# Optimization experiments

Hardware: AMD Instinct MI355X
Metric: run time of the kernel (lower is better)

The kernel has to match this reference:

```python
import jax, jax.numpy as jnp
import numpy as np

N = 50000   # nodes
D = 128     # input_dim
E = 1600000 # edges
K = 100     # out_nodes


def setup_inputs() -> dict:
    key = jax.random.key(0)
    ks = jax.random.split(key, 9)
    x = jax.random.normal(ks[0], (N, D), dtype=jnp.float32)
    edge_index = jax.random.randint(ks[1], (2, E), 0, N, dtype=jnp.int64)
    # PyG GCNConv params: Linear(in,out,bias=False) weight + separate bias
    s = 1.0 / np.sqrt(D)
    W1 = jax.random.uniform(ks[2], (D, D), jnp.float32, -s, s)
    b1 = jnp.zeros((D,), jnp.float32)
    W2 = jax.random.uniform(ks[3], (D, D), jnp.float32, -s, s)
    b2 = jnp.zeros((D,), jnp.float32)
    Wa = jax.random.uniform(ks[4], (D, K), jnp.float32, -s, s)
    ba = jax.random.uniform(ks[5], (K,), jnp.float32, -s, s)
    return {"x": x, "edge_index": edge_index, "W1": W1, "b1": b1,
            "W2": W2, "b2": b2, "Wa": Wa, "ba": ba}


def _gcn_conv(x, src, dst, norm, W, b, n_nodes):
    # PyG GCNConv: h = x @ W; aggregate D^-1/2 (A+I) D^-1/2 h; add bias
    h = x @ W                                  # [N, D]
    msg = h[src] * norm[:, None]               # [E+N, D] gather + scale
    agg = jax.ops.segment_sum(msg, dst, num_segments=n_nodes)  # scatter-add
    return agg + b


def reference(x, edge_index, W1, b1, W2, b2, Wa, ba):
    n = x.shape[0]
    loop = jnp.arange(n, dtype=edge_index.dtype)
    src = jnp.concatenate([edge_index[0], loop])   # add self-loops
    dst = jnp.concatenate([edge_index[1], loop])
    deg = jnp.zeros((n,), x.dtype).at[dst].add(1.0)
    dinv = jnp.where(deg > 0, jax.lax.rsqrt(deg), 0.0)
    norm = dinv[src] * dinv[dst]                   # [E+N]

    h = _gcn_conv(x, src, dst, norm, W1, b1, n)
    h = jax.nn.relu(h)
    h = _gcn_conv(h, src, dst, norm, W2, b2, n)
    s = jax.nn.softmax(h @ Wa + ba, axis=1)        # [N, K]
    return s
```

## Files before the change

kernel.cpp:

```cpp
#include <hip/hip_runtime.h>

#define D 128
#define KOUT 100
#define CHUNK 4096

typedef __attribute__((ext_vector_type(8))) short short8;
typedef __attribute__((ext_vector_type(4))) float floatx4;

__device__ inline float bf_lo(unsigned int u) { return __uint_as_float(u << 16); }
__device__ inline float bf_hi(unsigned int u) { return __uint_as_float(u & 0xFFFF0000u); }

__device__ inline unsigned int bf_round(float a) {
    unsigned int ua = __float_as_uint(a);
    return (ua + 0x7FFFu + ((ua >> 16) & 1u)) >> 16;
}
__device__ inline unsigned int pack_bf(float a, float b) {
    return bf_round(a) | (bf_round(b) << 16);
}


__launch_bounds__(256)
__global__ void bucket_pass1(const int* __restrict__ ei, int E, int nbuck, int cap,
                             int* __restrict__ bcur, unsigned int* __restrict__ bdata) {
    __shared__ int hist[256];
    __shared__ int sc[256];
    __shared__ int pfx[256];
    __shared__ int cur[256];
    __shared__ int gbase[256];
    __shared__ unsigned int lbuf[CHUNK];
    __shared__ unsigned char bkt[CHUNK];

    int tid = threadIdx.x;
    int base = blockIdx.x * CHUNK;
    int cnt = E - base; if (cnt > CHUNK) cnt = CHUNK;

    hist[tid] = 0;
    __syncthreads();

    int src[CHUNK / 256];
    int dst[CHUNK / 256];
#pragma unroll
    for (int q = 0; q < CHUNK / 256; q++) {
        int li = tid + q * 256;
        if (li < cnt) {
            src[q] = ei[base + li];
            dst[q] = ei[E + base + li];
            atomicAdd(&hist[dst[q] >> 8], 1);
        }
    }
    __syncthreads();

    int v = hist[tid];
    sc[tid] = v;
    __syncthreads();
    for (int off = 1; off < 256; off <<= 1) {
        int t = (tid >= off) ? sc[tid - off] : 0;
        __syncthreads();
        sc[tid] += t;
        __syncthreads();
    }
    int excl = sc[tid] - v;
    pfx[tid] = excl;
    cur[tid] = excl;
    gbase[tid] = 0;
    if (tid < nbuck && v > 0) gbase[tid] = atomicAdd(&bcur[tid], v);
    __syncthreads();

#pragma unroll
    for (int q = 0; q < CHUNK / 256; q++) {
        int li = tid + q * 256;
        if (li < cnt) {
            int b = dst[q] >> 8;
            int p = atomicAdd(&cur[b], 1);
            lbuf[p] = (unsigned int)src[q] | ((unsigned int)(dst[q] & 255) << 24);
            bkt[p] = (unsigned char)b;
        }
    }
    __syncthreads();

    for (int p = tid; p < cnt; p += 256) {
        int b = bkt[p];
        bdata[(size_t)b * cap + gbase[b] + (p - pfx[b])] = lbuf[p];
    }
}


__launch_bounds__(256)
__global__ void bucket_build(const unsigned int* __restrict__ bdata, const int* __restrict__ bcur,
                             int cap, float* __restrict__ dinv,
                             int* __restrict__ rowptr, int* __restrict__ csr, int n, int nbuck) {
    __shared__ int cnts[256];
    __shared__ int sc[256];
    __shared__ int cur[256];
    __shared__ int bbase;

    int b = blockIdx.x, tid = threadIdx.x;
    if (tid == 0) bbase = 0;
    cnts[tid] = 0;
    __syncthreads();

    int part = 0;
    for (int t = tid; t < b; t += 256) part += bcur[t];
#pragma unroll
    for (int off = 32; off > 0; off >>= 1) part += __shfl_down(part, off);
    if ((tid & 63) == 0 && part != 0) atomicAdd(&bbase, part);

    int cnt = bcur[b];
    const unsigned int* p = bdata + (size_t)b * cap;
    for (int e = tid; e < cnt; e += 256) atomicAdd(&cnts[p[e] >> 24], 1);
    __syncthreads();

    int v = cnts[tid];
    sc[tid] = v;
    __syncthreads();
    for (int off = 1; off < 256; off <<= 1) {
        int t = (tid >= off) ? sc[tid - off] : 0;
        __syncthreads();
        sc[tid] += t;
        __syncthreads();
    }
    int gstart = bbase + (sc[tid] - v);
    int node = b * 256 + tid;
    if (node < n) {
        dinv[node] = rsqrtf((float)(v + 1));
        rowptr[node] = gstart;
    }
    cur[tid] = gstart;
    __syncthreads();

    for (int e = tid; e < cnt; e += 256) {
        unsigned int u = p[e];
        int pos = atomicAdd(&cur[u >> 24], 1);
        csr[pos] = (int)(u & 0xFFFFFFu);
    }
}


__global__ void prep_frag_kernel(const float* __restrict__ W1, const float* __restrict__ W2,
                                 const float* __restrict__ Wa, const float* __restrict__ ba,
                                 unsigned short* __restrict__ Wf1, unsigned short* __restrict__ Wf2,
                                 unsigned short* __restrict__ WfA, float* __restrict__ bpad,
                                 int* __restrict__ bcur, int* __restrict__ rowptr,
                                 unsigned int* __restrict__ zrowA, unsigned int* __restrict__ zrowB,
                                 int n, int E) {
    int idx = blockIdx.x * blockDim.x + threadIdx.x;
    if (idx < 3 * 16384) {
        int m = idx / 16384;
        int e = idx & 16383;
        int j = e & 7, lane = (e >> 3) & 63, ct = (e >> 9) & 7, kt = e >> 12;
        int k = kt * 32 + (lane >> 4) * 8 + j;
        int col = ct * 16 + (lane & 15);
        float val;
        unsigned short* dst;
        if (m == 0)      { val = W1[k * 128 + col]; dst = Wf1; }
        else if (m == 1) { val = W2[k * 128 + col]; dst = Wf2; }
        else             { val = (col < KOUT) ? Wa[k * KOUT + col] : 0.f; dst = WfA; }
        dst[e] = (unsigned short)bf_round(val);
    }
    if (idx < 128) bpad[idx] = (idx < KOUT) ? ba[idx] : 0.f;
    if (idx < 256) bcur[idx] = 0;
    if (idx < 64) { zrowA[idx] = 0u; zrowB[idx] = 0u; }
    if (idx == 256) rowptr[n] = E;
}


__launch_bounds__(256)
__global__ void gemm_mfma_kernel(const void* __restrict__ Xin, const unsigned short* __restrict__ Wf,
                                 const float* __restrict__ bias, const float* __restrict__ oscale,
                                 void* __restrict__ Y, int nrows, int in_bf16, int out_mode) {
    __shared__ float lds_f[64 * 130];
    unsigned short* lds_h = (unsigned short*)lds_f;
    unsigned int* lds_u = (unsigned int*)lds_f;

    int tid = threadIdx.x;
    int w = tid >> 6, lane = tid & 63;
    int quad = lane >> 4, m16 = lane & 15;
    int r0 = blockIdx.x * 64;

    if (!in_bf16) {
        int row = tid >> 2, cg_ = tid & 3;
        bool valid = (r0 + row) < nrows;
        const float4* Xr = (const float4*)Xin + (size_t)(r0 + row) * 32 + cg_ * 8;
#pragma unroll
        for (int j = 0; j < 8; j++) {
            float4 v = valid ? Xr[j] : make_float4(0.f, 0.f, 0.f, 0.f);
            int c = cg_ * 32 + j * 4;
            lds_u[row * 68 + (c >> 1)]     = pack_bf(v.x, v.y);
            lds_u[row * 68 + (c >> 1) + 1] = pack_bf(v.z, v.w);
        }
        __syncthreads();
    }

    floatx4 acc[8];
#pragma unroll
    for (int ct = 0; ct < 8; ct++) acc[ct] = (floatx4){0.f, 0.f, 0.f, 0.f};

    int arow = r0 + w * 16 + m16;
    if (arow > nrows - 1) arow = nrows - 1;
    const unsigned int* Xb = (const unsigned int*)Xin;

    const short8* Wf8 = (const short8*)Wf;
#pragma unroll
    for (int kt = 0; kt < 4; kt++) {
        short8 a;
        if (in_bf16) {
            a = *(const short8*)(Xb + (size_t)arow * 64 + kt * 16 + quad * 4);
        } else {
            a = *(const short8*)(lds_h + (w * 16 + m16) * 136 + kt * 32 + quad * 8);
        }
#pragma unroll
        for (int ct = 0; ct < 8; ct++) {
            short8 b = Wf8[(kt * 8 + ct) * 64 + lane];
            acc[ct] = __builtin_amdgcn_mfma_f32_16x16x32_bf16(a, b, acc[ct], 0, 0, 0);
        }
    }

    if (out_mode == 1) {
        __syncthreads();
#pragma unroll
        for (int ct = 0; ct < 8; ct++) {
#pragma unroll
            for (int r = 0; r < 4; r++) {
                int rl = w * 16 + quad * 4 + r;
                lds_f[rl * 130 + ct * 16 + m16] = acc[ct][r];
            }
        }
        __syncthreads();
        unsigned int* Yb = (unsigned int*)Y;
        for (int r = 0; r < 16; r++) {
            int row = r0 + w * 16 + r;
            if (row < nrows) {
                float sc = oscale ? oscale[row] : 1.f;
                float lo = lds_f[(w * 16 + r) * 130 + 2 * lane] * sc;
                float hi = lds_f[(w * 16 + r) * 130 + 2 * lane + 1] * sc;
                Yb[(size_t)row * 64 + lane] = pack_bf(lo, hi);
            }
        }
    } else {
        float bb[8];
#pragma unroll
        for (int ct = 0; ct < 8; ct++) bb[ct] = bias[ct * 16 + m16];
        float* Yf = (float*)Y;
#pragma unroll
        for (int r = 0; r < 4; r++) {
            int row = r0 + w * 16 + quad * 4 + r;
            float vv[8];
            float mx = -1e30f;
#pragma unroll
            for (int ct = 0; ct < 8; ct++) {
                int col = ct * 16 + m16;
                vv[ct] = (col < KOUT) ? acc[ct][r] + bb[ct] : -1e30f;
                mx = fmaxf(mx, vv[ct]);
            }
#pragma unroll
            for (int off = 1; off < 16; off <<= 1) mx = fmaxf(mx, __shfl_xor(mx, off));
            float se = 0.f;
#pragma unroll
            for (int ct = 0; ct < 8; ct++) {
                vv[ct] = (vv[ct] > -1e29f) ? __expf(vv[ct] - mx) : 0.f;
                se += vv[ct];
            }
#pragma unroll
            for (int off = 1; off < 16; off <<= 1) se += __shfl_xor(se, off);
            float inv = 1.f / se;
            if (row < nrows) {
#pragma unroll
                for (int ct = 0; ct < 8; ct++) {
                    int col = ct * 16 + m16;
                    if (col < KOUT) Yf[(size_t)row * KOUT + col] = vv[ct] * inv;
                }
            }
        }
    }
}


__launch_bounds__(256)
__global__ void aggregate_kernel(const uint4* __restrict__ Hb4, const int* __restrict__ csr,
                                 const int* __restrict__ rowptr,
                                 const float* __restrict__ dinv, const float* __restrict__ bias,
                                 unsigned int* __restrict__ Ob, int n, int do_relu) {
    int wid = threadIdx.x >> 6, lane = threadIdx.x & 63;
    int g = lane >> 4, c = lane & 15;
    int i = blockIdx.x * 4 + wid;
    if (i >= n) return;

    float di = dinv[i];
    int start = rowptr[i];
    int cnt = rowptr[i + 1] - start;
    const int* cp = csr + start;

    float acc[8];
    {
        uint4 sv = Hb4[(size_t)i * 16 + c];
        unsigned int su[4] = {sv.x, sv.y, sv.z, sv.w};
        if (g != 0) { su[0] = su[1] = su[2] = su[3] = 0u; }
#pragma unroll
        for (int t = 0; t < 4; t++) {
            acc[2 * t]     = bf_lo(su[t]);
            acc[2 * t + 1] = bf_hi(su[t]);
        }
    }

    int s[4];
#pragma unroll
    for (int u = 0; u < 4; u++) {
        int idx = u * 4 + g;
        s[u] = (idx < cnt) ? cp[idx] : n;
    }
    for (int e = 0; e < cnt; e += 16) {
        uint4 v[4];
#pragma unroll
        for (int u = 0; u < 4; u++) v[u] = Hb4[(size_t)s[u] * 16 + c];
        int ns[4];
#pragma unroll
        for (int u = 0; u < 4; u++) {
            int idx = e + 16 + u * 4 + g;
            ns[u] = (idx < cnt) ? cp[idx] : n;
        }
#pragma unroll
        for (int u = 0; u < 4; u++) {
            unsigned int uu[4] = {v[u].x, v[u].y, v[u].z, v[u].w};
#pragma unroll
            for (int t = 0; t < 4; t++) {
                acc[2 * t]     += bf_lo(uu[t]);
                acc[2 * t + 1] += bf_hi(uu[t]);
            }
        }
#pragma unroll
        for (int u = 0; u < 4; u++) s[u] = ns[u];
    }

#pragma unroll
    for (int j = 0; j < 8; j++) {
        acc[j] += __shfl_xor(acc[j], 16);
        acc[j] += __shfl_xor(acc[j], 32);
    }

    float2 bb = ((const float2*)bias)[c * 4 + g];
    float fx = acc[g * 2]     * di + bb.x;
    float fy = acc[g * 2 + 1] * di + bb.y;
    if (do_relu) { fx = fmaxf(fx, 0.f); fy = fmaxf(fy, 0.f); }
    Ob[(size_t)i * 64 + c * 4 + g] = pack_bf(fx, fy);
}


extern "C" void kernel_launch(void* const* d_in, const int* in_sizes, int n_in,
                              void* d_out, int out_size, void* d_ws, size_t ws_size,
                              hipStream_t stream) {
    const float* x  = (const float*)d_in[0];
    const int*   ei = (const int*)d_in[1];
    const float* W1 = (const float*)d_in[2];
    const float* b1 = (const float*)d_in[3];
    const float* W2 = (const float*)d_in[4];
    const float* b2 = (const float*)d_in[5];
    const float* Wa = (const float*)d_in[6];
    const float* ba = (const float*)d_in[7];
    float* out = (float*)d_out;

    int N = in_sizes[0] / D;
    int E = in_sizes[1] / 2;

    int nbuck = (N + 255) >> 8;
    int cap = ((E / nbuck) + 2048 + 63) & ~63;

    char* w = (char*)d_ws;
    size_t off = 0;
    auto carve = [&](size_t bytes) -> void* {
        void* p = w + off;
        off = (off + bytes + 255) & ~(size_t)255;
        return p;
    };
    float* dinv   = (float*)carve((size_t)N * 4);
    int*   rowptr = (int*)carve((size_t)(N + 1) * 4);
    int*   bcur   = (int*)carve(256 * 4);
    unsigned int* bdata = (unsigned int*)carve((size_t)nbuck * cap * 4);
    int*   csr    = (int*)carve((size_t)E * 4);
    unsigned short* Wf1 = (unsigned short*)carve(16384 * 2);
    unsigned short* Wf2 = (unsigned short*)carve(16384 * 2);
    unsigned short* WfA = (unsigned short*)carve(16384 * 2);
    float* bpad   = (float*)carve(512);
    unsigned int* HbA = (unsigned int*)carve((size_t)(N + 1) * 64 * 4);
    unsigned int* HbB = (unsigned int*)carve((size_t)(N + 1) * 64 * 4);
    (void)ws_size; (void)n_in; (void)out_size;

    int nbNode4 = (N + 3) / 4;
    int nbGemm = (N + 63) / 64;
    int nbP1 = (E + CHUNK - 1) / CHUNK;

    prep_frag_kernel<<<192, 256, 0, stream>>>(W1, W2, Wa, ba, Wf1, Wf2, WfA, bpad,
                                              bcur, rowptr,
                                              HbA + (size_t)N * 64, HbB + (size_t)N * 64, N, E);
    bucket_pass1<<<nbP1, 256, 0, stream>>>(ei, E, nbuck, cap, bcur, bdata);
    bucket_build<<<nbuck, 256, 0, stream>>>(bdata, bcur, cap, dinv, rowptr, csr, N, nbuck);

    gemm_mfma_kernel<<<nbGemm, 256, 0, stream>>>(x, Wf1, nullptr, dinv, HbA, N, 0, 1);
    aggregate_kernel<<<nbNode4, 256, 0, stream>>>((const uint4*)HbA, csr, rowptr, dinv, b1, HbB, N, 1);
    gemm_mfma_kernel<<<nbGemm, 256, 0, stream>>>(HbB, Wf2, nullptr, dinv, HbA, N, 1, 1);
    aggregate_kernel<<<nbNode4, 256, 0, stream>>>((const uint4*)HbA, csr, rowptr, dinv, b2, HbB, N, 0);
    gemm_mfma_kernel<<<nbGemm, 256, 0, stream>>>(HbB, WfA, bpad, nullptr, out, N, 1, 2);
}
```

Baseline: 266.7 us.

## Fuse all GCN stages into one cooperative persistent kernel with grid syncs

Replaces the eight separate kernel launches with a single cooperative mega-kernel. The stages run as grid-stride phases on a persistent grid sized by occupancy (capped at 1024 blocks) and are separated by grid.sync(). The aggregate phase becomes a grid-stride loop over nodes that prefetches the next node's row pointers and computes dinv inline. The aim is to remove launch gaps and per-kernel tail effects. In exchange the grid is smaller, grid barriers add cost, and LDS sized for the largest phase may limit occupancy; separate kernels remain as a fallback if the cooperative launch fails.

```diff
diff --git a/kernel.cpp b/kernel.cpp
--- a/kernel.cpp
+++ b/kernel.cpp
@@ -1,11 +1,15 @@
 #include <hip/hip_runtime.h>
+#include <hip/hip_cooperative_groups.h>
 
 #define D 128
 #define KOUT 100
 #define CHUNK 4096
 
+namespace cg = cooperative_groups;
+
 typedef __attribute__((ext_vector_type(8))) short short8;
 typedef __attribute__((ext_vector_type(4))) float floatx4;
+typedef __attribute__((ext_vector_type(4))) unsigned int uintx4;
 
 __device__ inline float bf_lo(unsigned int u) { return __uint_as_float(u << 16); }
 __device__ inline float bf_hi(unsigned int u) { return __uint_as_float(u & 0xFFFF0000u); }
@@ -18,131 +22,18 @@
     return bf_round(a) | (bf_round(b) << 16);
 }
 
-
-__launch_bounds__(256)
-__global__ void bucket_pass1(const int* __restrict__ ei, int E, int nbuck, int cap,
-                             int* __restrict__ bcur, unsigned int* __restrict__ bdata) {
-    __shared__ int hist[256];
-    __shared__ int sc[256];
-    __shared__ int pfx[256];
-    __shared__ int cur[256];
-    __shared__ int gbase[256];
-    __shared__ unsigned int lbuf[CHUNK];
-    __shared__ unsigned char bkt[CHUNK];
-
-    int tid = threadIdx.x;
-    int base = blockIdx.x * CHUNK;
-    int cnt = E - base; if (cnt > CHUNK) cnt = CHUNK;
-
-    hist[tid] = 0;
-    __syncthreads();
-
-    int src[CHUNK / 256];
-    int dst[CHUNK / 256];
-#pragma unroll
-    for (int q = 0; q < CHUNK / 256; q++) {
-        int li = tid + q * 256;
-        if (li < cnt) {
-            src[q] = ei[base + li];
-            dst[q] = ei[E + base + li];
-            atomicAdd(&hist[dst[q] >> 8], 1);
-        }
-    }
-    __syncthreads();
-
-    int v = hist[tid];
-    sc[tid] = v;
-    __syncthreads();
-    for (int off = 1; off < 256; off <<= 1) {
-        int t = (tid >= off) ? sc[tid - off] : 0;
-        __syncthreads();
-        sc[tid] += t;
-        __syncthreads();
-    }
-    int excl = sc[tid] - v;
-    pfx[tid] = excl;
-    cur[tid] = excl;
-    gbase[tid] = 0;
-    if (tid < nbuck && v > 0) gbase[tid] = atomicAdd(&bcur[tid], v);
-    __syncthreads();
-
-#pragma unroll
-    for (int q = 0; q < CHUNK / 256; q++) {
-        int li = tid + q * 256;
-        if (li < cnt) {
-            int b = dst[q] >> 8;
-            int p = atomicAdd(&cur[b], 1);
-            lbuf[p] = (unsigned int)src[q] | ((unsigned int)(dst[q] & 255) << 24);
-            bkt[p] = (unsigned char)b;
-        }
-    }
-    __syncthreads();
-
-    for (int p = tid; p < cnt; p += 256) {
-        int b = bkt[p];
-        bdata[(size_t)b * cap + gbase[b] + (p - pfx[b])] = lbuf[p];
-    }
-}
-
-
-__launch_bounds__(256)
-__global__ void bucket_build(const unsigned int* __restrict__ bdata, const int* __restrict__ bcur,
-                             int cap, float* __restrict__ dinv,
-                             int* __restrict__ rowptr, int* __restrict__ csr, int n, int nbuck) {
-    __shared__ int cnts[256];
-    __shared__ int sc[256];
-    __shared__ int cur[256];
-    __shared__ int bbase;
-
-    int b = blockIdx.x, tid = threadIdx.x;
-    if (tid == 0) bbase = 0;
-    cnts[tid] = 0;
-    __syncthreads();
-
-    int part = 0;
-    for (int t = tid; t < b; t += 256) part += bcur[t];
-#pragma unroll
-    for (int off = 32; off > 0; off >>= 1) part += __shfl_down(part, off);
-    if ((tid & 63) == 0 && part != 0) atomicAdd(&bbase, part);
-
-    int cnt = bcur[b];
-    const unsigned int* p = bdata + (size_t)b * cap;
-    for (int e = tid; e < cnt; e += 256) atomicAdd(&cnts[p[e] >> 24], 1);
-    __syncthreads();
-
-    int v = cnts[tid];
-    sc[tid] = v;
-    __syncthreads();
-    for (int off = 1; off < 256; off <<= 1) {
-        int t = (tid >= off) ? sc[tid - off] : 0;
-        __syncthreads();
-        sc[tid] += t;
-        __syncthreads();
-    }
-    int gstart = bbase + (sc[tid] - v);
-    int node = b * 256 + tid;
-    if (node < n) {
-        dinv[node] = rsqrtf((float)(v + 1));
-        rowptr[node] = gstart;
-    }
-    cur[tid] = gstart;
-    __syncthreads();
-
-    for (int e = tid; e < cnt; e += 256) {
-        unsigned int u = p[e];
-        int pos = atomicAdd(&cur[u >> 24], 1);
-        csr[pos] = (int)(u & 0xFFFFFFu);
-    }
-}
-
-
-__global__ void prep_frag_kernel(const float* __restrict__ W1, const float* __restrict__ W2,
-                                 const float* __restrict__ Wa, const float* __restrict__ ba,
-                                 unsigned short* __restrict__ Wf1, unsigned short* __restrict__ Wf2,
-                                 unsigned short* __restrict__ WfA, float* __restrict__ bpad,
-                                 int* __restrict__ bcur, int* __restrict__ rowptr,
-                                 unsigned int* __restrict__ zrowA, unsigned int* __restrict__ zrowB,
-                                 int n, int E) {
+struct MegaArgs {
+    const float* x; const int* ei;
+    const float* W1; const float* b1; const float* W2; const float* b2;
+    const float* Wa; const float* ba;
+    float* out;
+    float* dinv; int* rowptr; int* bcur; unsigned int* bdata; int* csr;
+    unsigned short* Wf1; unsigned short* Wf2; unsigned short* WfA; float* bpad;
+    unsigned int* HbA; unsigned int* HbB;
+    int N, E, nbuck, cap, nbP1, nbGemm;
+};
+
+__device__ void prep_body(const MegaArgs& A) {
     int idx = blockIdx.x * blockDim.x + threadIdx.x;
     if (idx < 3 * 16384) {
         int m = idx / 16384;
@@ -152,198 +43,366 @@
         int col = ct * 16 + (lane & 15);
         float val;
         unsigned short* dst;
-        if (m == 0)      { val = W1[k * 128 + col]; dst = Wf1; }
-        else if (m == 1) { val = W2[k * 128 + col]; dst = Wf2; }
-        else             { val = (col < KOUT) ? Wa[k * KOUT + col] : 0.f; dst = WfA; }
+        if (m == 0)      { val = A.W1[k * 128 + col]; dst = A.Wf1; }
+        else if (m == 1) { val = A.W2[k * 128 + col]; dst = A.Wf2; }
+        else             { val = (col < KOUT) ? A.Wa[k * KOUT + col] : 0.f; dst = A.WfA; }
         dst[e] = (unsigned short)bf_round(val);
     }
-    if (idx < 128) bpad[idx] = (idx < KOUT) ? ba[idx] : 0.f;
-    if (idx < 256) bcur[idx] = 0;
-    if (idx < 64) { zrowA[idx] = 0u; zrowB[idx] = 0u; }
-    if (idx == 256) rowptr[n] = E;
-}
-
-
-__launch_bounds__(256)
-__global__ void gemm_mfma_kernel(const void* __restrict__ Xin, const unsigned short* __restrict__ Wf,
-                                 const float* __restrict__ bias, const float* __restrict__ oscale,
-                                 void* __restrict__ Y, int nrows, int in_bf16, int out_mode) {
-    __shared__ float lds_f[64 * 130];
+    if (idx < 128) A.bpad[idx] = (idx < KOUT) ? A.ba[idx] : 0.f;
+    if (idx < 256) A.bcur[idx] = 0;
+    if (idx < 64) {
+        A.HbA[(size_t)A.N * 64 + idx] = 0u;
+        A.HbB[(size_t)A.N * 64 + idx] = 0u;
+    }
+    if (idx == 256) A.rowptr[A.N] = A.E;
+}
+
+__device__ void pass1_phase(const MegaArgs& A, float* lds) {
+    int* hist = (int*)lds;
+    int* sc   = hist + 256;
+    int* pfx  = sc + 256;
+    int* cur  = pfx + 256;
+    int* gbase = cur + 256;
+    unsigned int* lbuf = (unsigned int*)(gbase + 256);
+    unsigned char* bkt = (unsigned char*)(lbuf + CHUNK);
+
+    int tid = threadIdx.x;
+    for (int ch = blockIdx.x; ch < A.nbP1; ch += gridDim.x) {
+        int base = ch * CHUNK;
+        int cnt = A.E - base; if (cnt > CHUNK) cnt = CHUNK;
+
+        __syncthreads();
+        hist[tid] = 0;
+        __syncthreads();
+
+        int src[CHUNK / 256];
+        int dst[CHUNK / 256];
+#pragma unroll
+        for (int q = 0; q < CHUNK / 256; q++) {
+            int li = tid + q * 256;
+            if (li < cnt) {
+                src[q] = A.ei[base + li];
+                dst[q] = A.ei[A.E + base + li];
+                atomicAdd(&hist[dst[q] >> 8], 1);
+            }
+        }
+        __syncthreads();
+
+        int v = hist[tid];
+        sc[tid] = v;
+        __syncthreads();
+        for (int off = 1; off < 256; off <<= 1) {
+            int t = (tid >= off) ? sc[tid - off] : 0;
+            __syncthreads();
+            sc[tid] += t;
+            __syncthreads();
+        }
+        int excl = sc[tid] - v;
+        pfx[tid] = excl;
+        cur[tid] = excl;
+        gbase[tid] = 0;
+        if (tid < A.nbuck && v > 0) gbase[tid] = atomicAdd(&A.bcur[tid], v);
+        __syncthreads();
+
+#pragma unroll
+        for (int q = 0; q < CHUNK / 256; q++) {
+            int li = tid + q * 256;
+            if (li < cnt) {
+                int b = dst[q] >> 8;
+                int p = atomicAdd(&cur[b], 1);
+                lbuf[p] = (unsigned int)src[q] | ((unsigned int)(dst[q] & 255) << 24);
+                bkt[p] = (unsigned char)b;
+            }
+        }
+        __syncthreads();
+
+        for (int p = tid; p < cnt; p += 256) {
+            int b = bkt[p];
+            A.bdata[(size_t)b * A.cap + gbase[b] + (p - pfx[b])] = lbuf[p];
+        }
+    }
+}
+
+__device__ void build_phase(const MegaArgs& A, float* lds) {
+    int* cnts = (int*)lds;
+    int* sc   = cnts + 256;
+    int* cur  = sc + 256;
+    int* pbb  = cur + 256;
+
+    int tid = threadIdx.x;
+    for (int b = blockIdx.x; b < A.nbuck; b += gridDim.x) {
+        __syncthreads();
+        if (tid == 0) pbb[0] = 0;
+        cnts[tid] = 0;
+        __syncthreads();
+
+        int part = 0;
+        for (int t = tid; t < b; t += 256) part += A.bcur[t];
+#pragma unroll
+        for (int off = 32; off > 0; off >>= 1) part += __shfl_down(part, off);
+        if ((tid & 63) == 0 && part != 0) atomicAdd(&pbb[0], part);
+
+        int cnt = A.bcur[b];
+        const unsigned int* p = A.bdata + (size_t)b * A.cap;
+        for (int e = tid; e < cnt; e += 256) atomicAdd(&cnts[p[e] >> 24], 1);
+        __syncthreads();
+
+        int v = cnts[tid];
+        sc[tid] = v;
+        __syncthreads();
+        for (int off = 1; off < 256; off <<= 1) {
+            int t = (tid >= off) ? sc[tid - off] : 0;
+            __syncthreads();
+            sc[tid] += t;
+            __syncthreads();
+        }
+        int gstart = pbb[0] + (sc[tid] - v);
+        int node = b * 256 + tid;
+        if (node < A.N) {
+            A.dinv[node] = rsqrtf((float)(v + 1));
+            A.rowptr[node] = gstart;
+        }
+        cur[tid] = gstart;
+        __syncthreads();
+
+        for (int e = tid; e < cnt; e += 256) {
+            unsigned int u = p[e];
+            int pos = atomicAdd(&cur[u >> 24], 1);
+            A.csr[pos] = (int)(u & 0xFFFFFFu);
+        }
+    }
+}
+
+__device__ void gemm_phase(const void* Xin, const unsigned short* Wf,
+                           const float* bias, const float* oscale,
+                           void* Y, int nrows, int in_bf16, int out_mode,
+                           float* lds_f, int ntiles) {
     unsigned short* lds_h = (unsigned short*)lds_f;
     unsigned int* lds_u = (unsigned int*)lds_f;
 
     int tid = threadIdx.x;
     int w = tid >> 6, lane = tid & 63;
     int quad = lane >> 4, m16 = lane & 15;
-    int r0 = blockIdx.x * 64;
-
-    if (!in_bf16) {
-        int row = tid >> 2, cg_ = tid & 3;
-        bool valid = (r0 + row) < nrows;
-        const float4* Xr = (const float4*)Xin + (size_t)(r0 + row) * 32 + cg_ * 8;
-#pragma unroll
-        for (int j = 0; j < 8; j++) {
-            float4 v = valid ? Xr[j] : make_float4(0.f, 0.f, 0.f, 0.f);
-            int c = cg_ * 32 + j * 4;
-            lds_u[row * 68 + (c >> 1)]     = pack_bf(v.x, v.y);
-            lds_u[row * 68 + (c >> 1) + 1] = pack_bf(v.z, v.w);
-        }
-        __syncthreads();
-    }
-
-    floatx4 acc[8];
-#pragma unroll
-    for (int ct = 0; ct < 8; ct++) acc[ct] = (floatx4){0.f, 0.f, 0.f, 0.f};
-
-    int arow = r0 + w * 16 + m16;
-    if (arow > nrows - 1) arow = nrows - 1;
-    const unsigned int* Xb = (const unsigned int*)Xin;
-
-    const short8* Wf8 = (const short8*)Wf;
-#pragma unroll
-    for (int kt = 0; kt < 4; kt++) {
-        short8 a;
-        if (in_bf16) {
-            a = *(const short8*)(Xb + (size_t)arow * 64 + kt * 16 + quad * 4);
+
+    for (int t = blockIdx.x; t < ntiles; t += gridDim.x) {
+        int r0 = t * 64;
+
+        if (!in_bf16) {
+            int row = tid >> 2, cg_ = tid & 3;
+            bool valid = (r0 + row) < nrows;
+            const float4* Xr = (const float4*)Xin + (size_t)(r0 + row) * 32 + cg_ * 8;
+#pragma unroll
+            for (int j = 0; j < 8; j++) {
+                float4 v = valid ? Xr[j] : make_float4(0.f, 0.f, 0.f, 0.f);
+                int c = cg_ * 32 + j * 4;
+                lds_u[row * 68 + (c >> 1)]     = pack_bf(v.x, v.y);
+                lds_u[row * 68 + (c >> 1) + 1] = pack_bf(v.z, v.w);
+            }
+            __syncthreads();
+        }
+
+        floatx4 acc[8];
+#pragma unroll
+        for (int ct = 0; ct < 8; ct++) acc[ct] = (floatx4){0.f, 0.f, 0.f, 0.f};
+
+        int arow = r0 + w * 16 + m16;
+        if (arow > nrows - 1) arow = nrows - 1;
+        const unsigned int* Xb = (const unsigned int*)Xin;
+
+        const short8* Wf8 = (const short8*)Wf;
+#pragma unroll
+        for (int kt = 0; kt < 4; kt++) {
+            short8 a;
+            if (in_bf16) {
+                a = *(const short8*)(Xb + (size_t)arow * 64 + kt * 16 + quad * 4);
+            } else {
+                a = *(const short8*)(lds_h + (w * 16 + m16) * 136 + kt * 32 + quad * 8);
+            }
+#pragma unroll
+            for (int ct = 0; ct < 8; ct++) {
+                short8 b = Wf8[(kt * 8 + ct) * 64 + lane];
+                acc[ct] = __builtin_amdgcn_mfma_f32_16x16x32_bf16(a, b, acc[ct], 0, 0, 0);
+            }
+        }
+
+        if (out_mode == 1) {
+            __syncthreads();
+#pragma unroll
+            for (int ct = 0; ct < 8; ct++) {
+#pragma unroll
+                for (int r = 0; r < 4; r++) {
+                    int rl = w * 16 + quad * 4 + r;
+                    lds_f[rl * 130 + ct * 16 + m16] = acc[ct][r];
+                }
+            }
+            __syncthreads();
+            unsigned int* Yb = (unsigned int*)Y;
+            for (int r = 0; r < 16; r++) {
+                int row = r0 + w * 16 + r;
+                if (row < nrows) {
+                    float sc = oscale ? oscale[row] : 1.f;
+                    float lo = lds_f[(w * 16 + r) * 130 + 2 * lane] * sc;
+                    float hi = lds_f[(w * 16 + r) * 130 + 2 * lane + 1] * sc;
+                    Yb[(size_t)row * 64 + lane] = pack_bf(lo, hi);
+                }
+            }
         } else {
-            a = *(const short8*)(lds_h + (w * 16 + m16) * 136 + kt * 32 + quad * 8);
-        }
-#pragma unroll
-        for (int ct = 0; ct < 8; ct++) {
-            short8 b = Wf8[(kt * 8 + ct) * 64 + lane];
-            acc[ct] = __builtin_amdgcn_mfma_f32_16x16x32_bf16(a, b, acc[ct], 0, 0, 0);
-        }
-    }
-
-    if (out_mode == 1) {
-        __syncthreads();
-#pragma unroll
-        for (int ct = 0; ct < 8; ct++) {
+            float bb[8];
+#pragma unroll
+            for (int ct = 0; ct < 8; ct++) bb[ct] = bias[ct * 16 + m16];
+            float* Yf = (float*)Y;
 #pragma unroll
             for (int r = 0; r < 4; r++) {
-                int rl = w * 16 + quad * 4 + r;
-                lds_f[rl * 130 + ct * 16 + m16] = acc[ct][r];
-            }
-        }
-        __syncthreads();
-        unsigned int* Yb = (unsigned int*)Y;
-        for (int r = 0; r < 16; r++) {
-            int row = r0 + w * 16 + r;
-            if (row < nrows) {
-                float sc = oscale ? oscale[row] : 1.f;
-                float lo = lds_f[(w * 16 + r) * 130 + 2 * lane] * sc;
-                float hi = lds_f[(w * 16 + r) * 130 + 2 * lane + 1] * sc;
-                Yb[(size_t)row * 64 + lane] = pack_bf(lo, hi);
-            }
-        }
-    } else {
-        float bb[8];
-#pragma unroll
-        for (int ct = 0; ct < 8; ct++) bb[ct] = bias[ct * 16 + m16];
-        float* Yf = (float*)Y;
-#pragma unroll
-        for (int r = 0; r < 4; r++) {
-            int row = r0 + w * 16 + quad * 4 + r;
-            float vv[8];
-            float mx = -1e30f;
-#pragma unroll
-            for (int ct = 0; ct < 8; ct++) {
-                int col = ct * 16 + m16;
-                vv[ct] = (col < KOUT) ? acc[ct][r] + bb[ct] : -1e30f;
-                mx = fmaxf(mx, vv[ct]);
-            }
-#pragma unroll
-            for (int off = 1; off < 16; off <<= 1) mx = fmaxf(mx, __shfl_xor(mx, off));
-            float se = 0.f;
-#pragma unroll
-            for (int ct = 0; ct < 8; ct++) {
-                vv[ct] = (vv[ct] > -1e29f) ? __expf(vv[ct] - mx) : 0.f;
-                se += vv[ct];
-            }
-#pragma unroll
-            for (int off = 1; off < 16; off <<= 1) se += __shfl_xor(se, off);
-            float inv = 1.f / se;
-            if (row < nrows) {
+                int row = r0 + w * 16 + quad * 4 + r;
+                float vv[8];
+                float mx = -1e30f;
 #pragma unroll
                 for (int ct = 0; ct < 8; ct++) {
                     int col = ct * 16 + m16;
-                    if (col < KOUT) Yf[(size_t)row * KOUT + col] = vv[ct] * inv;
+                    vv[ct] = (col < KOUT) ? acc[ct][r] + bb[ct] : -1e30f;
+                    mx = fmaxf(mx, vv[ct]);
                 }
-            }
-        }
-    }
-}
-
-
-__launch_bounds__(256)
-__global__ void aggregate_kernel(const uint4* __restrict__ Hb4, const int* __restrict__ csr,
-                                 const int* __restrict__ rowptr,
-                                 const float* __restrict__ dinv, const float* __restrict__ bias,
-                                 unsigned int* __restrict__ Ob, int n, int do_relu) {
+#pragma unroll
+                for (int off = 1; off < 16; off <<= 1) mx = fmaxf(mx, __shfl_xor(mx, off));
+                float se = 0.f;
+#pragma unroll
+                for (int ct = 0; ct < 8; ct++) {
+                    vv[ct] = (vv[ct] > -1e29f) ? __expf(vv[ct] - mx) : 0.f;
+                    se += vv[ct];
+                }
+#pragma unroll
+                for (int off = 1; off < 16; off <<= 1) se += __shfl_xor(se, off);
+                float inv = 1.f / se;
+                if (row < nrows) {
+#pragma unroll
+                    for (int ct = 0; ct < 8; ct++) {
+                        int col = ct * 16 + m16;
+                        if (col < KOUT) Yf[(size_t)row * KOUT + col] = vv[ct] * inv;
+                    }
+                }
+            }
+        }
+        __syncthreads();
+    }
+}
+
+__device__ void agg_phase(const unsigned int* __restrict__ Hb, const int* __restrict__ csr,
+                          const int* __restrict__ rowptr, const float* __restrict__ bias,
+                          unsigned int* __restrict__ Ob, int n, int do_relu) {
     int wid = threadIdx.x >> 6, lane = threadIdx.x & 63;
     int g = lane >> 4, c = lane & 15;
-    int i = blockIdx.x * 4 + wid;
-    if (i >= n) return;
-
-    float di = dinv[i];
-    int start = rowptr[i];
-    int cnt = rowptr[i + 1] - start;
-    const int* cp = csr + start;
-
-    float acc[8];
-    {
-        uint4 sv = Hb4[(size_t)i * 16 + c];
-        unsigned int su[4] = {sv.x, sv.y, sv.z, sv.w};
-        if (g != 0) { su[0] = su[1] = su[2] = su[3] = 0u; }
-#pragma unroll
-        for (int t = 0; t < 4; t++) {
-            acc[2 * t]     = bf_lo(su[t]);
-            acc[2 * t + 1] = bf_hi(su[t]);
-        }
-    }
-
-    int s[4];
-#pragma unroll
-    for (int u = 0; u < 4; u++) {
-        int idx = u * 4 + g;
-        s[u] = (idx < cnt) ? cp[idx] : n;
-    }
-    for (int e = 0; e < cnt; e += 16) {
-        uint4 v[4];
-#pragma unroll
-        for (int u = 0; u < 4; u++) v[u] = Hb4[(size_t)s[u] * 16 + c];
-        int ns[4];
+    int wgid = blockIdx.x * 4 + wid;
+    int wstride = gridDim.x * 4;
+    const char* Tb = (const char*)Hb;
+    unsigned coff = (unsigned)c * 16u;
+
+    int i = wgid;
+    int start = 0, cnt = 0;
+    if (i < n) { start = rowptr[i]; cnt = rowptr[i + 1] - start; }
+
+    while (i < n) {
+        int inext = i + wstride;
+        int nstart = 0, ncnt = 0;
+        if (inext < n) { nstart = rowptr[inext]; ncnt = rowptr[inext + 1] - nstart; }
+
+        const int* cp = csr + start;
+        float di = rsqrtf((float)(cnt + 1));
+
+        float acc[8];
+        {
+            uintx4 sv = (uintx4){0u, 0u, 0u, 0u};
+            if (g == 0) sv = *(const uintx4*)(Tb + (unsigned)i * 256u + coff);
+            acc[0] = bf_lo(sv.x); acc[1] = bf_hi(sv.x);
+            acc[2] = bf_lo(sv.y); acc[3] = bf_hi(sv.y);
+            acc[4] = bf_lo(sv.z); acc[5] = bf_hi(sv.z);
+            acc[6] = bf_lo(sv.w); acc[7] = bf_hi(sv.w);
+        }
+
+        int s[4];
 #pragma unroll
         for (int u = 0; u < 4; u++) {
-            int idx = e + 16 + u * 4 + g;
-            ns[u] = (idx < cnt) ? cp[idx] : n;
-        }
-#pragma unroll
-        for (int u = 0; u < 4; u++) {
-            unsigned int uu[4] = {v[u].x, v[u].y, v[u].z, v[u].w};
-#pragma unroll
-            for (int t = 0; t < 4; t++) {
-                acc[2 * t]     += bf_lo(uu[t]);
-                acc[2 * t + 1] += bf_hi(uu[t]);
-            }
-        }
-#pragma unroll
-        for (int u = 0; u < 4; u++) s[u] = ns[u];
-    }
-
-#pragma unroll
-    for (int j = 0; j < 8; j++) {
-        acc[j] += __shfl_xor(acc[j], 16);
-        acc[j] += __shfl_xor(acc[j], 32);
-    }
-
-    float2 bb = ((const float2*)bias)[c * 4 + g];
-    float fx = acc[g * 2]     * di + bb.x;
-    float fy = acc[g * 2 + 1] * di + bb.y;
-    if (do_relu) { fx = fmaxf(fx, 0.f); fy = fmaxf(fy, 0.f); }
-    Ob[(size_t)i * 64 + c * 4 + g] = pack_bf(fx, fy);
-}
-
+            int idx = u * 4 + g;
+            s[u] = (idx < cnt) ? cp[idx] : n;
+        }
+        for (int e = 0; e < cnt; e += 16) {
+            uintx4 v[4];
+#pragma unroll
+            for (int u = 0; u < 4; u++)
+                v[u] = *(const uintx4*)(Tb + (unsigned)s[u] * 256u + coff);
+            int ns[4];
+#pragma unroll
+            for (int u = 0; u < 4; u++) {
+                int idx = e + 16 + u * 4 + g;
+                ns[u] = (idx < cnt) ? cp[idx] : n;
+            }
+#pragma unroll
+            for (int u = 0; u < 4; u++) {
+                acc[0] += bf_lo(v[u].x); acc[1] += bf_hi(v[u].x);
+                acc[2] += bf_lo(v[u].y); acc[3] += bf_hi(v[u].y);
+                acc[4] += bf_lo(v[u].z); acc[5] += bf_hi(v[u].z);
+                acc[6] += bf_lo(v[u].w); acc[7] += bf_hi(v[u].w);
+            }
+#pragma unroll
+            for (int u = 0; u < 4; u++) s[u] = ns[u];
+        }
+
+#pragma unroll
+        for (int j = 0; j < 8; j++) {
+            acc[j] += __shfl_xor(acc[j], 16);
+            acc[j] += __shfl_xor(acc[j], 32);
+        }
+
+        float2 bb = ((const float2*)bias)[c * 4 + g];
+        float fx = acc[g * 2]     * di + bb.x;
+        float fy = acc[g * 2 + 1] * di + bb.y;
+        if (do_relu) { fx = fmaxf(fx, 0.f); fy = fmaxf(fy, 0.f); }
+        Ob[(size_t)i * 64 + c * 4 + g] = pack_bf(fx, fy);
+
+        i = inext; start = nstart; cnt = ncnt;
+    }
+}
+
+__launch_bounds__(256, 4)
+__global__ void mega_kernel(MegaArgs A) {
+    __shared__ float lds_f[64 * 130];
+    cg::grid_group grid = cg::this_grid();
+
+    prep_body(A);
+    grid.sync();
+    pass1_phase(A, lds_f);
+    grid.sync();
+    build_phase(A, lds_f);
+    grid.sync();
+    gemm_phase(A.x, A.Wf1, nullptr, A.dinv, A.HbA, A.N, 0, 1, lds_f, A.nbGemm);
+    grid.sync();
+    agg_phase(A.HbA, A.csr, A.rowptr, A.b1, A.HbB, A.N, 1);
+    grid.sync();
+    gemm_phase(A.HbB, A.Wf2, nullptr, A.dinv, A.HbA, A.N, 1, 1, lds_f, A.nbGemm);
+    grid.sync();
+    agg_phase(A.HbA, A.csr, A.rowptr, A.b2, A.HbB, A.N, 0);
+    grid.sync();
+    gemm_phase(A.HbB, A.WfA, A.bpad, nullptr, A.out, A.N, 1, 2, lds_f, A.nbGemm);
+}
+
+__launch_bounds__(256) __global__ void k_prep(MegaArgs A) { prep_body(A); }
+__launch_bounds__(256) __global__ void k_pass1(MegaArgs A) {
+    __shared__ float lds[64 * 130]; pass1_phase(A, lds);
+}
+__launch_bounds__(256) __global__ void k_build(MegaArgs A) {
+    __shared__ float lds[64 * 130]; build_phase(A, lds);
+}
+__launch_bounds__(256) __global__ void k_gemm(const void* Xin, const unsigned short* Wf,
+                                              const float* bias, const float* oscale,
+                                              void* Y, int nrows, int in_bf16, int out_mode,
+                                              int ntiles) {
+    __shared__ float lds[64 * 130];
+    gemm_phase(Xin, Wf, bias, oscale, Y, nrows, in_bf16, out_mode, lds, ntiles);
+}
+__launch_bounds__(256) __global__ void k_agg(const unsigned int* Hb, const int* csr,
+                                             const int* rowptr, const float* bias,
+                                             unsigned int* Ob, int n, int do_relu) {
+    agg_phase(Hb, csr, rowptr, bias, Ob, n, do_relu);
+}
 
 extern "C" void kernel_launch(void* const* d_in, const int* in_sizes, int n_in,
                               void* d_out, int out_size, void* d_ws, size_t ws_size,
@@ -384,19 +443,35 @@
     unsigned int* HbB = (unsigned int*)carve((size_t)(N + 1) * 64 * 4);
     (void)ws_size; (void)n_in; (void)out_size;
 
-    int nbNode4 = (N + 3) / 4;
-    int nbGemm = (N + 63) / 64;
-    int nbP1 = (E + CHUNK - 1) / CHUNK;
-
-    prep_frag_kernel<<<192, 256, 0, stream>>>(W1, W2, Wa, ba, Wf1, Wf2, WfA, bpad,
-                                              bcur, rowptr,
-                                              HbA + (size_t)N * 64, HbB + (size_t)N * 64, N, E);
-    bucket_pass1<<<nbP1, 256, 0, stream>>>(ei, E, nbuck, cap, bcur, bdata);
-    bucket_build<<<nbuck, 256, 0, stream>>>(bdata, bcur, cap, dinv, rowptr, csr, N, nbuck);
-
-    gemm_mfma_kernel<<<nbGemm, 256, 0, stream>>>(x, Wf1, nullptr, dinv, HbA, N, 0, 1);
-    aggregate_kernel<<<nbNode4, 256, 0, stream>>>((const uint4*)HbA, csr, rowptr, dinv, b1, HbB, N, 1);
-    gemm_mfma_kernel<<<nbGemm, 256, 0, stream>>>(HbB, Wf2, nullptr, dinv, HbA, N, 1, 1);
-    aggregate_kernel<<<nbNode4, 256, 0, stream>>>((const uint4*)HbA, csr, rowptr, dinv, b2, HbB, N, 0);
-    gemm_mfma_kernel<<<nbGemm, 256, 0, stream>>>(HbB, WfA, bpad, nullptr, out, N, 1, 2);
-}
+    MegaArgs a;
+    a.x = x; a.ei = ei; a.W1 = W1; a.b1 = b1; a.W2 = W2; a.b2 = b2;
+    a.Wa = Wa; a.ba = ba; a.out = out;
+    a.dinv = dinv; a.rowptr = rowptr; a.bcur = bcur; a.bdata = bdata; a.csr = csr;
+    a.Wf1 = Wf1; a.Wf2 = Wf2; a.WfA = WfA; a.bpad = bpad;
+    a.HbA = HbA; a.HbB = HbB;
+    a.N = N; a.E = E; a.nbuck = nbuck; a.cap = cap;
+    a.nbP1 = (E + CHUNK - 1) / CHUNK;
+    a.nbGemm = (N + 63) / 64;
+
+    int occ = 0;
+    hipError_t oe = hipOccupancyMaxActiveBlocksPerMultiprocessor(
+        &occ, (const void*)mega_kernel, 256, 0);
+    if (oe != hipSuccess || occ < 1) occ = 1;
+    int grid = occ * 256;
+    if (grid > 1024) grid = 1024;
+
+    void* kp[] = { (void*)&a };
+    hipError_t err = hipLaunchCooperativeKernel((const void*)mega_kernel,
+                                                dim3(grid), dim3(256), kp, 0, stream);
+    if (err != hipSuccess) {
+        int nbNode4 = (N + 3) / 4;
+        k_prep<<<192, 256, 0, stream>>>(a);
+        k_pass1<<<a.nbP1, 256, 0, stream>>>(a);
+        k_build<<<nbuck, 256, 0, stream>>>(a);
+        k_gemm<<<a.nbGemm, 256, 0, stream>>>(x, Wf1, nullptr, dinv, HbA, N, 0, 1, a.nbGemm);
+        k_agg<<<nbNode4, 256, 0, stream>>>(HbA, csr, rowptr, b1, HbB, N, 1);
+        k_gemm<<<a.nbGemm, 256, 0, stream>>>(HbB, Wf2, nullptr, dinv, HbA, N, 1, 1, a.nbGemm);
+        k_agg<<<nbNode4, 256, 0, stream>>>(HbA, csr, rowptr, b2, HbB, N, 0);
+        k_gemm<<<a.nbGemm, 256, 0, stream>>>(HbB, WfA, bpad, nullptr, out, N, 1, 2, a.nbGemm);
+    }
+}
```

After: 642.6 us. 141% more time.

## Fold W2 into classifier weight and drop the second GEMM

Applied to the files above, without the earlier changes.

The second GCN layer's linear transform is moved past its aggregation using associativity: aggregate(h)·W2·Wa equals aggregate(h)·(W2·Wa). The product W2·Wa and the folded bias b2·Wa+ba are computed in the prep kernel. The first aggregation now also applies the source-side dinv scale, and the second aggregation runs without bias on the relu output. This removes one full N×128×128 GEMM pass and its HBM round trip. In exchange the prep kernel does a small serial 128-term dot product per weight element, and the folded weights are rounded to bf16, which changes rounding slightly.

```diff
diff --git a/kernel.cpp b/kernel.cpp
--- a/kernel.cpp
+++ b/kernel.cpp
@@ -138,26 +138,41 @@
 
 __global__ void prep_frag_kernel(const float* __restrict__ W1, const float* __restrict__ W2,
                                  const float* __restrict__ Wa, const float* __restrict__ ba,
-                                 unsigned short* __restrict__ Wf1, unsigned short* __restrict__ Wf2,
-                                 unsigned short* __restrict__ WfA, float* __restrict__ bpad,
+                                 const float* __restrict__ b2,
+                                 unsigned short* __restrict__ Wf1, unsigned short* __restrict__ WfF,
+                                 float* __restrict__ bpad,
                                  int* __restrict__ bcur, int* __restrict__ rowptr,
                                  unsigned int* __restrict__ zrowA, unsigned int* __restrict__ zrowB,
                                  int n, int E) {
     int idx = blockIdx.x * blockDim.x + threadIdx.x;
-    if (idx < 3 * 16384) {
-        int m = idx / 16384;
+    if (idx < 2 * 16384) {
+        int m = idx >> 14;
         int e = idx & 16383;
         int j = e & 7, lane = (e >> 3) & 63, ct = (e >> 9) & 7, kt = e >> 12;
         int k = kt * 32 + (lane >> 4) * 8 + j;
         int col = ct * 16 + (lane & 15);
-        float val;
-        unsigned short* dst;
-        if (m == 0)      { val = W1[k * 128 + col]; dst = Wf1; }
-        else if (m == 1) { val = W2[k * 128 + col]; dst = Wf2; }
-        else             { val = (col < KOUT) ? Wa[k * KOUT + col] : 0.f; dst = WfA; }
-        dst[e] = (unsigned short)bf_round(val);
-    }
-    if (idx < 128) bpad[idx] = (idx < KOUT) ? ba[idx] : 0.f;
+        if (m == 0) {
+            Wf1[e] = (unsigned short)bf_round(W1[k * 128 + col]);
+        } else {
+            float s = 0.f;
+            if (col < KOUT) {
+                const float* w2r = W2 + k * 128;
+#pragma unroll 8
+                for (int mm = 0; mm < 128; mm++)
+                    s = fmaf(w2r[mm], Wa[mm * KOUT + col], s);
+            }
+            WfF[e] = (unsigned short)bf_round(s);
+        }
+    }
+    if (idx < 128) {
+        float s = 0.f;
+        if (idx < KOUT) {
+            for (int mm = 0; mm < 128; mm++)
+                s = fmaf(b2[mm], Wa[mm * KOUT + idx], s);
+            s += ba[idx];
+        }
+        bpad[idx] = s;
+    }
     if (idx < 256) bcur[idx] = 0;
     if (idx < 64) { zrowA[idx] = 0u; zrowB[idx] = 0u; }
     if (idx == 256) rowptr[n] = E;
@@ -279,7 +294,7 @@
 __global__ void aggregate_kernel(const uint4* __restrict__ Hb4, const int* __restrict__ csr,
                                  const int* __restrict__ rowptr,
                                  const float* __restrict__ dinv, const float* __restrict__ bias,
-                                 unsigned int* __restrict__ Ob, int n, int do_relu) {
+                                 unsigned int* __restrict__ Ob, int n, int do_relu, int post_scale) {
     int wid = threadIdx.x >> 6, lane = threadIdx.x & 63;
     int g = lane >> 4, c = lane & 15;
     int i = blockIdx.x * 4 + wid;
@@ -337,10 +352,11 @@
         acc[j] += __shfl_xor(acc[j], 32);
     }
 
-    float2 bb = ((const float2*)bias)[c * 4 + g];
+    float2 bb = bias ? ((const float2*)bias)[c * 4 + g] : make_float2(0.f, 0.f);
     float fx = acc[g * 2]     * di + bb.x;
     float fy = acc[g * 2 + 1] * di + bb.y;
     if (do_relu) { fx = fmaxf(fx, 0.f); fy = fmaxf(fy, 0.f); }
+    if (post_scale) { fx *= di; fy *= di; }
     Ob[(size_t)i * 64 + c * 4 + g] = pack_bf(fx, fy);
 }
 
@@ -377,8 +393,7 @@
     unsigned int* bdata = (unsigned int*)carve((size_t)nbuck * cap * 4);
     int*   csr    = (int*)carve((size_t)E * 4);
     unsigned short* Wf1 = (unsigned short*)carve(16384 * 2);
-    unsigned short* Wf2 = (unsigned short*)carve(16384 * 2);
-    unsigned short* WfA = (unsigned short*)carve(16384 * 2);
+    unsigned short* WfF = (unsigned short*)carve(16384 * 2);
     float* bpad   = (float*)carve(512);
     unsigned int* HbA = (unsigned int*)carve((size_t)(N + 1) * 64 * 4);
     unsigned int* HbB = (unsigned int*)carve((size_t)(N + 1) * 64 * 4);
@@ -388,15 +403,14 @@
     int nbGemm = (N + 63) / 64;
     int nbP1 = (E + CHUNK - 1) / CHUNK;
 
-    prep_frag_kernel<<<192, 256, 0, stream>>>(W1, W2, Wa, ba, Wf1, Wf2, WfA, bpad,
+    prep_frag_kernel<<<128, 256, 0, stream>>>(W1, W2, Wa, ba, b2, Wf1, WfF, bpad,
                                               bcur, rowptr,
                                               HbA + (size_t)N * 64, HbB + (size_t)N * 64, N, E);
     bucket_pass1<<<nbP1, 256, 0, stream>>>(ei, E, nbuck, cap, bcur, bdata);
     bucket_build<<<nbuck, 256, 0, stream>>>(bdata, bcur, cap, dinv, rowptr, csr, N, nbuck);
 
     gemm_mfma_kernel<<<nbGemm, 256, 0, stream>>>(x, Wf1, nullptr, dinv, HbA, N, 0, 1);
-    aggregate_kernel<<<nbNode4, 256, 0, stream>>>((const uint4*)HbA, csr, rowptr, dinv, b1, HbB, N, 1);
-    gemm_mfma_kernel<<<nbGemm, 256, 0, stream>>>(HbB, Wf2, nullptr, dinv, HbA, N, 1, 1);
-    aggregate_kernel<<<nbNode4, 256, 0, stream>>>((const uint4*)HbA, csr, rowptr, dinv, b2, HbB, N, 0);
-    gemm_mfma_kernel<<<nbGemm, 256, 0, stream>>>(HbB, WfA, bpad, nullptr, out, N, 1, 2);
-}
+    aggregate_kernel<<<nbNode4, 256, 0, stream>>>((const uint4*)HbA, csr, rowptr, dinv, b1, HbB, N, 1, 1);
+    aggregate_kernel<<<nbNode4, 256, 0, stream>>>((const uint4*)HbB, csr, rowptr, dinv, nullptr, HbA, N, 0, 0);
+    gemm_mfma_kernel<<<nbGemm, 256, 0, stream>>>(HbA, WfF, bpad, nullptr, out, N, 1, 2);
+}
```

After: 254.8 us. 1.05x faster.
